# Kernel tuning notes

Measured on AMD Instinct MI355X. Metric: run time of the kernel, lower is better.

Reference implementation:

```python
import jax, jax.numpy as jnp
import numpy as np

N_NODES = 100000


def setup_inputs() -> dict:
    key = jax.random.key(0)
    k1, k2, k3 = jax.random.split(key, 3)
    x = jax.random.normal(k1, (N_NODES, 128), dtype=jnp.float32)
    edge_index = jax.random.randint(k2, (2, 500000), 0, N_NODES, dtype=jnp.int64)
    # GCNConv linear weight (glorot-ish scale) and bias
    W = jax.random.normal(k3, (128, 512), dtype=jnp.float32) * (1.0 / np.sqrt(128.0))
    b = jnp.zeros((512,), dtype=jnp.float32)
    prelu_w = jnp.full((512,), 0.25, dtype=jnp.float32)  # torch PReLU default init
    return {"x": x, "edge_index": edge_index, "W": W, "b": b, "prelu_w": prelu_w}


def reference(x, edge_index, W, b, prelu_w):
    N = x.shape[0]
    # 1) linear transform (GCNConv applies lin before aggregation, bias after)
    h = x @ W  # [N, H]
    # 2) add self-loops
    loops = jnp.arange(N, dtype=edge_index.dtype)
    src = jnp.concatenate([edge_index[0], loops])  # [E+N]
    dst = jnp.concatenate([edge_index[1], loops])
    # 3) symmetric normalization: deg computed on destination nodes
    deg = jax.ops.segment_sum(jnp.ones_like(src, dtype=h.dtype), dst, num_segments=N)
    dinv = jnp.where(deg > 0, deg ** -0.5, 0.0)
    norm = dinv[src] * dinv[dst]  # [E+N]
    # 4) normalized scatter-add aggregation
    msg = h[src] * norm[:, None]  # [E+N, H]
    out = jax.ops.segment_sum(msg, dst, num_segments=N) + b  # [N, H]
    # 5) channel-wise PReLU
    return jnp.where(out >= 0, out, prelu_w * out)
```

## Files before the change

### kernel.cpp

```cpp
#include <hip/hip_runtime.h>


typedef __attribute__((ext_vector_type(8))) short bf16x8_t;
typedef __attribute__((ext_vector_type(4))) float f32x4;

#define N_NODES 100000
#define N_EDGES 500000
#define K_IN    128
#define H_OUT   512
#define MAXDEG  32
#define NEB     1954

static __device__ __forceinline__ unsigned short f2b(float f) {
    unsigned u = __float_as_uint(f);
    u = (u + 0x7FFFu + ((u >> 16) & 1u)) >> 16;
    return (unsigned short)u;
}
static __device__ __forceinline__ float b2lo(unsigned v) {
    return __uint_as_float(v << 16);
}
static __device__ __forceinline__ float b2hi(unsigned v) {
    return __uint_as_float(v & 0xFFFF0000u);
}

__global__ __launch_bounds__(256) void k1(const int* __restrict__ ei,
                                          int* __restrict__ deg,
                                          int* __restrict__ csrp,
                                          const float* __restrict__ W,
                                          unsigned short* __restrict__ Wt) {
    int b = blockIdx.x;
    if (b < NEB) {
        int e = b * 256 + threadIdx.x;
        if (e < N_EDGES) {
            int s = ei[e];
            int d = ei[N_EDGES + e];
            int r = atomicAdd(&deg[d], 1);
            csrp[d * MAXDEG + r] = s;
        }
    } else {
        int i = (b - NEB) * 256 + threadIdx.x;
        int n = i >> 7, k = i & 127;
        Wt[i] = f2b(W[k * H_OUT + n]);
    }
}

__global__ __launch_bounds__(256) void k2(const int* __restrict__ deg,
                                          const float* __restrict__ x,
                                          unsigned* __restrict__ xs) {
    int i = blockIdx.x * 256 + threadIdx.x;
    int row = i >> 6;
    float d = rsqrtf((float)(deg[row] + 1));
    const float2* x2 = (const float2*)x;
    float2 xv = x2[i];
    xs[i] = ((unsigned)f2b(d * xv.y) << 16) | f2b(d * xv.x);
}

__global__ __launch_bounds__(256) void k5(const unsigned* __restrict__ xs,
                                          const int* __restrict__ csrp,
                                          const int* __restrict__ deg,
                                          unsigned* __restrict__ xa) {
    int wave = threadIdx.x >> 6, lane = threadIdx.x & 63;
    int node = blockIdx.x * 4 + wave;
    if (node >= N_NODES) return;

    unsigned sv = xs[(size_t)node * 64 + lane];
    float a0 = b2lo(sv), a1 = b2hi(sv);

    int cnt = __builtin_amdgcn_readfirstlane(deg[node]);
    int base = node * MAXDEG;

    for (int j = 0; j < cnt; j += 8) {
        unsigned v[8];
        #pragma unroll
        for (int t = 0; t < 8; ++t) {
            int valid = (j + t < cnt);
            int idx = valid ? csrp[base + j + t] : 0;
            v[t] = valid ? xs[(size_t)idx * 64 + lane] : 0u;
        }
        #pragma unroll
        for (int t = 0; t < 8; ++t) { a0 += b2lo(v[t]); a1 += b2hi(v[t]); }
    }
    float di = rsqrtf((float)(cnt + 1));
    xa[(size_t)node * 64 + lane] = ((unsigned)f2b(di * a1) << 16) | f2b(di * a0);
}

__global__ __launch_bounds__(256) void k6(const unsigned short* __restrict__ xa,
                                          const unsigned short* __restrict__ Wt,
                                          const float* __restrict__ bias,
                                          const float* __restrict__ pw,
                                          float* __restrict__ out) {
    __shared__ char smem[65536];
    uint4* sA = (uint4*)smem;
    uint4* sB = (uint4*)(smem + 32768);
    float* ep = (float*)smem;

    int orig = blockIdx.x;
    int xcd = orig & 7, loc = orig >> 3;
    int wgid = (xcd < 4 ? xcd * 196 : 784 + (xcd - 4) * 195) + loc;
    const int n0 = (wgid & 3) * 128;
    const int mpair = wgid >> 2;
    const int tid = threadIdx.x;

    const uint4* A4 = (const uint4*)xa;
    const uint4* B4 = (const uint4*)Wt;

    #pragma unroll
    for (int r = 0; r < 8; ++r) {
        int i = tid + r * 256;
        int row = i >> 4, c = i & 15;
        sB[row * 16 + (c ^ (row & 7))] = B4[(size_t)(n0 + row) * 16 + c];
    }

    const int lane = tid & 63, wave = tid >> 6;
    const int wr = wave >> 1, wc = wave & 1;
    const int l16 = lane & 15, lq = lane >> 4;

    float bn[4], pn[4];
    #pragma unroll
    for (int n = 0; n < 4; ++n) {
        int gn = n0 + wc * 64 + n * 16 + l16;
        bn[n] = bias[gn];
        pn[n] = pw[gn];
    }

    for (int half = 0; half < 2; ++half) {
        const int m0 = (mpair * 2 + half) * 128;

        #pragma unroll
        for (int r = 0; r < 8; ++r) {
            int i = tid + r * 256;
            int row = i >> 4, c = i & 15;
            int grow = m0 + row;
            uint4 o = (grow < N_NODES) ? A4[(size_t)grow * 16 + c]
                                       : make_uint4(0u, 0u, 0u, 0u);
            sA[row * 16 + (c ^ (row & 7))] = o;
        }
        __syncthreads();

        f32x4 acc[4][4];
        #pragma unroll
        for (int m = 0; m < 4; ++m)
            #pragma unroll
            for (int n = 0; n < 4; ++n)
                acc[m][n] = (f32x4){0.f, 0.f, 0.f, 0.f};

        #pragma unroll
        for (int kk = 0; kk < 4; ++kk) {
            bf16x8_t av[4], bv[4];
            #pragma unroll
            for (int m = 0; m < 4; ++m) {
                int row = wr * 64 + m * 16 + l16;
                av[m] = __builtin_bit_cast(bf16x8_t, sA[row * 16 + ((kk * 4 + lq) ^ (row & 7))]);
            }
            #pragma unroll
            for (int n = 0; n < 4; ++n) {
                int row = wc * 64 + n * 16 + l16;
                bv[n] = __builtin_bit_cast(bf16x8_t, sB[row * 16 + ((kk * 4 + lq) ^ (row & 7))]);
            }
            #pragma unroll
            for (int m = 0; m < 4; ++m)
                #pragma unroll
                for (int n = 0; n < 4; ++n)
                    acc[m][n] = __builtin_amdgcn_mfma_f32_16x16x32_bf16(av[m], bv[n], acc[m][n], 0, 0, 0);
        }
        __syncthreads();

        #pragma unroll
        for (int h = 0; h < 2; ++h) {
            if (wr == h) {
                #pragma unroll
                for (int m = 0; m < 4; ++m)
                    #pragma unroll
                    for (int r = 0; r < 4; ++r) {
                        int row = m * 16 + lq * 4 + r;
                        #pragma unroll
                        for (int n = 0; n < 4; ++n) {
                            float t = acc[m][n][r] + bn[n];
                            float v = t >= 0.f ? t : pn[n] * t;
                            ep[row * 128 + wc * 64 + n * 16 + l16] = v;
                        }
                    }
            }
            __syncthreads();
            #pragma unroll
            for (int it = 0; it < 8; ++it) {
                int row = it * 8 + (tid >> 5);
                int gm = m0 + h * 64 + row;
                if (gm < N_NODES) {
                    int c4 = tid & 31;
                    f32x4 v = *(const f32x4*)&ep[row * 128 + c4 * 4];
                    __builtin_nontemporal_store(v, (f32x4*)&out[(size_t)gm * H_OUT + n0 + c4 * 4]);
                }
            }
            __syncthreads();
        }
    }
}

extern "C" void kernel_launch(void* const* d_in, const int* in_sizes, int n_in,
                              void* d_out, int out_size, void* d_ws, size_t ws_size,
                              hipStream_t stream) {
    const float* x    = (const float*)d_in[0];
    const int*   ei   = (const int*)d_in[1];
    const float* W    = (const float*)d_in[2];
    const float* bias = (const float*)d_in[3];
    const float* pw   = (const float*)d_in[4];
    float* out = (float*)d_out;

    char* ws = (char*)d_ws;
    size_t off = 0;
    auto alloc = [&](size_t bytes) -> void* {
        void* p = ws + off;
        off += (bytes + 255) & ~(size_t)255;
        return p;
    };
    unsigned*       xs   = (unsigned*)alloc((size_t)N_NODES * K_IN * 2);
    unsigned*       xa   = (unsigned*)alloc((size_t)N_NODES * K_IN * 2);
    unsigned short* Wt   = (unsigned short*)alloc((size_t)K_IN * H_OUT * 2);
    int*            deg  = (int*)alloc((size_t)N_NODES * 4);
    int*            csrp = (int*)alloc((size_t)N_NODES * MAXDEG * 4);
    (void)ws_size; (void)in_sizes; (void)n_in; (void)out_size;

    hipMemsetAsync(deg, 0, (size_t)N_NODES * 4, stream);

    k1 <<<NEB + 256, 256, 0, stream>>>(ei, deg, csrp, W, Wt);
    k2 <<<25000, 256, 0, stream>>>(deg, x, xs);
    k5 <<<(N_NODES + 3) / 4, 256, 0, stream>>>(xs, csrp, deg, xa);
    k6 <<<1564, 256, 0, stream>>>((const unsigned short*)xa,
                                  (const unsigned short*)Wt, bias, pw, out);
}
```

Baseline: 157.7 us.

## Fuse neighbor aggregation into the GEMM kernel via shared-memory A tile

Merges the gather/aggregate kernel and the GEMM+PReLU kernel into one 512-thread kernel. Each block aggregates 128 nodes straight into a swizzled shared-memory A tile, then loops over four 128-column output chunks, reloading the W tile each time. This removes the xa intermediate round trip through global memory and one launch. In exchange there are only 782 blocks, the gather and MFMA phases no longer overlap across kernels, and the epilogue now does scalar non-temporal stores instead of staged 16-byte vector stores.

```diff
diff --git a/kernel.cpp b/kernel.cpp
--- a/kernel.cpp
+++ b/kernel.cpp
@@ -10,6 +10,7 @@
 #define H_OUT   512
 #define MAXDEG  32
 #define NEB     1954
+#define NMT     782
 
 static __device__ __forceinline__ unsigned short f2b(float f) {
     unsigned u = __float_as_uint(f);
@@ -55,145 +56,118 @@
     xs[i] = ((unsigned)f2b(d * xv.y) << 16) | f2b(d * xv.x);
 }
 
-__global__ __launch_bounds__(256) void k5(const unsigned* __restrict__ xs,
-                                          const int* __restrict__ csrp,
-                                          const int* __restrict__ deg,
-                                          unsigned* __restrict__ xa) {
-    int wave = threadIdx.x >> 6, lane = threadIdx.x & 63;
-    int node = blockIdx.x * 4 + wave;
-    if (node >= N_NODES) return;
-
-    unsigned sv = xs[(size_t)node * 64 + lane];
-    float a0 = b2lo(sv), a1 = b2hi(sv);
-
-    int cnt = __builtin_amdgcn_readfirstlane(deg[node]);
-    int base = node * MAXDEG;
-
-    for (int j = 0; j < cnt; j += 8) {
-        unsigned v[8];
-        #pragma unroll
-        for (int t = 0; t < 8; ++t) {
-            int valid = (j + t < cnt);
-            int idx = valid ? csrp[base + j + t] : 0;
-            v[t] = valid ? xs[(size_t)idx * 64 + lane] : 0u;
-        }
-        #pragma unroll
-        for (int t = 0; t < 8; ++t) { a0 += b2lo(v[t]); a1 += b2hi(v[t]); }
-    }
-    float di = rsqrtf((float)(cnt + 1));
-    xa[(size_t)node * 64 + lane] = ((unsigned)f2b(di * a1) << 16) | f2b(di * a0);
-}
-
-__global__ __launch_bounds__(256) void k6(const unsigned short* __restrict__ xa,
-                                          const unsigned short* __restrict__ Wt,
-                                          const float* __restrict__ bias,
-                                          const float* __restrict__ pw,
-                                          float* __restrict__ out) {
+__global__ __launch_bounds__(512) void k56(const unsigned* __restrict__ xs,
+                                           const int* __restrict__ csrp,
+                                           const int* __restrict__ deg,
+                                           const unsigned short* __restrict__ Wt,
+                                           const float* __restrict__ bias,
+                                           const float* __restrict__ pw,
+                                           float* __restrict__ out) {
     __shared__ char smem[65536];
     uint4* sA = (uint4*)smem;
     uint4* sB = (uint4*)(smem + 32768);
-    float* ep = (float*)smem;
 
     int orig = blockIdx.x;
     int xcd = orig & 7, loc = orig >> 3;
-    int wgid = (xcd < 4 ? xcd * 196 : 784 + (xcd - 4) * 195) + loc;
-    const int n0 = (wgid & 3) * 128;
-    const int mpair = wgid >> 2;
+    int wgid = (xcd < 6 ? xcd * 98 : 588 + (xcd - 6) * 97) + loc;
+    const int m0 = wgid * 128;
     const int tid = threadIdx.x;
-
-    const uint4* A4 = (const uint4*)xa;
+    const int wave = tid >> 6, lane = tid & 63;
+
+    unsigned* sAd = (unsigned*)smem;
+    for (int i = 0; i < 16; ++i) {
+        int node = m0 + wave * 16 + i;
+        float a0 = 0.f, a1 = 0.f;
+        int cnt = 0;
+        if (node < N_NODES) {
+            unsigned sv = xs[(size_t)node * 64 + lane];
+            a0 = b2lo(sv); a1 = b2hi(sv);
+            cnt = __builtin_amdgcn_readfirstlane(deg[node]);
+            int base = node * MAXDEG;
+            for (int j = 0; j < cnt; j += 8) {
+                unsigned v[8];
+                #pragma unroll
+                for (int t = 0; t < 8; ++t) {
+                    int valid = (j + t < cnt);
+                    int idx = valid ? csrp[base + j + t] : 0;
+                    v[t] = valid ? xs[(size_t)idx * 64 + lane] : 0u;
+                }
+                #pragma unroll
+                for (int t = 0; t < 8; ++t) { a0 += b2lo(v[t]); a1 += b2hi(v[t]); }
+            }
+        }
+        float di = rsqrtf((float)(cnt + 1));
+        unsigned pk = ((unsigned)f2b(di * a1) << 16) | f2b(di * a0);
+        int row = wave * 16 + i;
+        int c = lane >> 2;
+        sAd[row * 64 + ((c ^ (row & 7)) << 2) + (lane & 3)] = pk;
+    }
+    __syncthreads();
+
     const uint4* B4 = (const uint4*)Wt;
-
-    #pragma unroll
-    for (int r = 0; r < 8; ++r) {
-        int i = tid + r * 256;
-        int row = i >> 4, c = i & 15;
-        sB[row * 16 + (c ^ (row & 7))] = B4[(size_t)(n0 + row) * 16 + c];
-    }
-
-    const int lane = tid & 63, wave = tid >> 6;
-    const int wr = wave >> 1, wc = wave & 1;
+    const int wr = wave >> 2, wc = wave & 3;
     const int l16 = lane & 15, lq = lane >> 4;
 
-    float bn[4], pn[4];
-    #pragma unroll
-    for (int n = 0; n < 4; ++n) {
-        int gn = n0 + wc * 64 + n * 16 + l16;
-        bn[n] = bias[gn];
-        pn[n] = pw[gn];
-    }
-
-    for (int half = 0; half < 2; ++half) {
-        const int m0 = (mpair * 2 + half) * 128;
-
-        #pragma unroll
-        for (int r = 0; r < 8; ++r) {
-            int i = tid + r * 256;
+    for (int nc = 0; nc < 4; ++nc) {
+        #pragma unroll
+        for (int r = 0; r < 4; ++r) {
+            int i = tid + r * 512;
             int row = i >> 4, c = i & 15;
-            int grow = m0 + row;
-            uint4 o = (grow < N_NODES) ? A4[(size_t)grow * 16 + c]
-                                       : make_uint4(0u, 0u, 0u, 0u);
-            sA[row * 16 + (c ^ (row & 7))] = o;
+            sB[row * 16 + (c ^ (row & 7))] = B4[(size_t)(nc * 128 + row) * 16 + c];
         }
         __syncthreads();
 
-        f32x4 acc[4][4];
+        f32x4 acc[4][2];
         #pragma unroll
         for (int m = 0; m < 4; ++m)
             #pragma unroll
-            for (int n = 0; n < 4; ++n)
+            for (int n = 0; n < 2; ++n)
                 acc[m][n] = (f32x4){0.f, 0.f, 0.f, 0.f};
 
         #pragma unroll
         for (int kk = 0; kk < 4; ++kk) {
-            bf16x8_t av[4], bv[4];
+            bf16x8_t av[4], bv[2];
             #pragma unroll
             for (int m = 0; m < 4; ++m) {
                 int row = wr * 64 + m * 16 + l16;
                 av[m] = __builtin_bit_cast(bf16x8_t, sA[row * 16 + ((kk * 4 + lq) ^ (row & 7))]);
             }
             #pragma unroll
-            for (int n = 0; n < 4; ++n) {
-                int row = wc * 64 + n * 16 + l16;
+            for (int n = 0; n < 2; ++n) {
+                int row = wc * 32 + n * 16 + l16;
                 bv[n] = __builtin_bit_cast(bf16x8_t, sB[row * 16 + ((kk * 4 + lq) ^ (row & 7))]);
             }
             #pragma unroll
             for (int m = 0; m < 4; ++m)
                 #pragma unroll
-                for (int n = 0; n < 4; ++n)
+                for (int n = 0; n < 2; ++n)
                     acc[m][n] = __builtin_amdgcn_mfma_f32_16x16x32_bf16(av[m], bv[n], acc[m][n], 0, 0, 0);
         }
+
+        float bn[2], pn[2];
+        #pragma unroll
+        for (int n = 0; n < 2; ++n) {
+            int gn = nc * 128 + wc * 32 + n * 16 + l16;
+            bn[n] = bias[gn];
+            pn[n] = pw[gn];
+        }
+        #pragma unroll
+        for (int m = 0; m < 4; ++m) {
+            #pragma unroll
+            for (int r = 0; r < 4; ++r) {
+                int gm = m0 + wr * 64 + m * 16 + lq * 4 + r;
+                if (gm < N_NODES) {
+                    #pragma unroll
+                    for (int n = 0; n < 2; ++n) {
+                        int gn = nc * 128 + wc * 32 + n * 16 + l16;
+                        float t = acc[m][n][r] + bn[n];
+                        float v = t >= 0.f ? t : pn[n] * t;
+                        __builtin_nontemporal_store(v, &out[(size_t)gm * H_OUT + gn]);
+                    }
+                }
+            }
+        }
         __syncthreads();
-
-        #pragma unroll
-        for (int h = 0; h < 2; ++h) {
-            if (wr == h) {
-                #pragma unroll
-                for (int m = 0; m < 4; ++m)
-                    #pragma unroll
-                    for (int r = 0; r < 4; ++r) {
-                        int row = m * 16 + lq * 4 + r;
-                        #pragma unroll
-                        for (int n = 0; n < 4; ++n) {
-                            float t = acc[m][n][r] + bn[n];
-                            float v = t >= 0.f ? t : pn[n] * t;
-                            ep[row * 128 + wc * 64 + n * 16 + l16] = v;
-                        }
-                    }
-            }
-            __syncthreads();
-            #pragma unroll
-            for (int it = 0; it < 8; ++it) {
-                int row = it * 8 + (tid >> 5);
-                int gm = m0 + h * 64 + row;
-                if (gm < N_NODES) {
-                    int c4 = tid & 31;
-                    f32x4 v = *(const f32x4*)&ep[row * 128 + c4 * 4];
-                    __builtin_nontemporal_store(v, (f32x4*)&out[(size_t)gm * H_OUT + n0 + c4 * 4]);
-                }
-            }
-            __syncthreads();
-        }
     }
 }
 
@@ -215,7 +189,6 @@
         return p;
     };
     unsigned*       xs   = (unsigned*)alloc((size_t)N_NODES * K_IN * 2);
-    unsigned*       xa   = (unsigned*)alloc((size_t)N_NODES * K_IN * 2);
     unsigned short* Wt   = (unsigned short*)alloc((size_t)K_IN * H_OUT * 2);
     int*            deg  = (int*)alloc((size_t)N_NODES * 4);
     int*            csrp = (int*)alloc((size_t)N_NODES * MAXDEG * 4);
@@ -225,7 +198,6 @@
 
     k1 <<<NEB + 256, 256, 0, stream>>>(ei, deg, csrp, W, Wt);
     k2 <<<25000, 256, 0, stream>>>(deg, x, xs);
-    k5 <<<(N_NODES + 3) / 4, 256, 0, stream>>>(xs, csrp, deg, xa);
-    k6 <<<1564, 256, 0, stream>>>((const unsigned short*)xa,
-                                  (const unsigned short*)Wt, bias, pw, out);
-}
+    k56<<<NMT, 512, 0, stream>>>(xs, csrp, deg,
+                                 (const unsigned short*)Wt, bias, pw, out);
+}
```

New measurement: 180.4 us. 14.4% more time.

## Process two nodes per wave in gather and store GEMM output directly

Applied to the files above, without the earlier changes.

The aggregation kernel now handles two destination nodes per wave, loading CSR neighbor indices as int4 vectors and issuing both nodes' gathers together to raise memory-level parallelism. Out-of-range indices are clamped and masked rather than branched on. Separately, the GEMM epilogue drops the LDS staging pass and its barriers and writes each scalar result straight to global memory with nontemporal stores. The direct epilogue produces narrower, less coalesced 4-byte stores (16 contiguous floats per row segment) in place of 16-byte vector stores, and the CSR loop reads padded slots that may hold uninitialized indices, which are clamped before use.

```diff
diff --git a/kernel.cpp b/kernel.cpp
--- a/kernel.cpp
+++ b/kernel.cpp
@@ -60,28 +60,52 @@
                                           const int* __restrict__ deg,
                                           unsigned* __restrict__ xa) {
     int wave = threadIdx.x >> 6, lane = threadIdx.x & 63;
-    int node = blockIdx.x * 4 + wave;
-    if (node >= N_NODES) return;
-
-    unsigned sv = xs[(size_t)node * 64 + lane];
-    float a0 = b2lo(sv), a1 = b2hi(sv);
-
-    int cnt = __builtin_amdgcn_readfirstlane(deg[node]);
-    int base = node * MAXDEG;
-
-    for (int j = 0; j < cnt; j += 8) {
-        unsigned v[8];
+    int n0 = blockIdx.x * 8 + wave * 2;
+    int n1 = n0 + 1;
+
+    unsigned sv0 = xs[(size_t)n0 * 64 + lane];
+    unsigned sv1 = xs[(size_t)n1 * 64 + lane];
+    int cnt0 = __builtin_amdgcn_readfirstlane(deg[n0]);
+    int cnt1 = __builtin_amdgcn_readfirstlane(deg[n1]);
+    float a00 = b2lo(sv0), a01 = b2hi(sv0);
+    float a10 = b2lo(sv1), a11 = b2hi(sv1);
+
+    const int4* cp0 = (const int4*)(csrp + n0 * MAXDEG);
+    const int4* cp1 = (const int4*)(csrp + n1 * MAXDEG);
+    int cmax = cnt0 > cnt1 ? cnt0 : cnt1;
+
+    for (int j = 0; j < cmax; j += 8) {
+        int4 ca0 = cp0[(j >> 2)];
+        int4 cb0 = cp0[(j >> 2) + 1];
+        int4 ca1 = cp1[(j >> 2)];
+        int4 cb1 = cp1[(j >> 2) + 1];
+        unsigned i0[8] = {(unsigned)ca0.x, (unsigned)ca0.y, (unsigned)ca0.z, (unsigned)ca0.w,
+                          (unsigned)cb0.x, (unsigned)cb0.y, (unsigned)cb0.z, (unsigned)cb0.w};
+        unsigned i1[8] = {(unsigned)ca1.x, (unsigned)ca1.y, (unsigned)ca1.z, (unsigned)ca1.w,
+                          (unsigned)cb1.x, (unsigned)cb1.y, (unsigned)cb1.z, (unsigned)cb1.w};
+        unsigned v0[8], v1[8];
         #pragma unroll
         for (int t = 0; t < 8; ++t) {
-            int valid = (j + t < cnt);
-            int idx = valid ? csrp[base + j + t] : 0;
-            v[t] = valid ? xs[(size_t)idx * 64 + lane] : 0u;
-        }
-        #pragma unroll
-        for (int t = 0; t < 8; ++t) { a0 += b2lo(v[t]); a1 += b2hi(v[t]); }
-    }
-    float di = rsqrtf((float)(cnt + 1));
-    xa[(size_t)node * 64 + lane] = ((unsigned)f2b(di * a1) << 16) | f2b(di * a0);
+            unsigned id0 = i0[t] < N_NODES ? i0[t] : 0u;
+            unsigned id1 = i1[t] < N_NODES ? i1[t] : 0u;
+            v0[t] = xs[(size_t)id0 * 64 + lane];
+            v1[t] = xs[(size_t)id1 * 64 + lane];
+        }
+        int rem0 = cnt0 - j, rem1 = cnt1 - j;
+        #pragma unroll
+        for (int t = 0; t < 8; ++t) {
+            unsigned w0 = (t < rem0) ? v0[t] : 0u;
+            unsigned w1 = (t < rem1) ? v1[t] : 0u;
+            a00 += b2lo(w0); a01 += b2hi(w0);
+            a10 += b2lo(w1); a11 += b2hi(w1);
+        }
+    }
+    float d0 = rsqrtf((float)(cnt0 + 1));
+    float d1 = rsqrtf((float)(cnt1 + 1));
+    unsigned p0 = ((unsigned)f2b(d0 * a01) << 16) | f2b(d0 * a00);
+    unsigned p1 = ((unsigned)f2b(d1 * a11) << 16) | f2b(d1 * a10);
+    __builtin_nontemporal_store(p0, &xa[(size_t)n0 * 64 + lane]);
+    __builtin_nontemporal_store(p1, &xa[(size_t)n1 * 64 + lane]);
 }
 
 __global__ __launch_bounds__(256) void k6(const unsigned short* __restrict__ xa,
@@ -92,7 +116,6 @@
     __shared__ char smem[65536];
     uint4* sA = (uint4*)smem;
     uint4* sB = (uint4*)(smem + 32768);
-    float* ep = (float*)smem;
 
     int orig = blockIdx.x;
     int xcd = orig & 7, loc = orig >> 3;
@@ -125,6 +148,7 @@
 
     for (int half = 0; half < 2; ++half) {
         const int m0 = (mpair * 2 + half) * 128;
+        if (half) __syncthreads();
 
         #pragma unroll
         for (int r = 0; r < 8; ++r) {
@@ -163,36 +187,22 @@
                 for (int n = 0; n < 4; ++n)
                     acc[m][n] = __builtin_amdgcn_mfma_f32_16x16x32_bf16(av[m], bv[n], acc[m][n], 0, 0, 0);
         }
-        __syncthreads();
-
-        #pragma unroll
-        for (int h = 0; h < 2; ++h) {
-            if (wr == h) {
-                #pragma unroll
-                for (int m = 0; m < 4; ++m)
+
+        #pragma unroll
+        for (int m = 0; m < 4; ++m) {
+            #pragma unroll
+            for (int r = 0; r < 4; ++r) {
+                int gm = m0 + wr * 64 + m * 16 + lq * 4 + r;
+                if (gm < N_NODES) {
                     #pragma unroll
-                    for (int r = 0; r < 4; ++r) {
-                        int row = m * 16 + lq * 4 + r;
-                        #pragma unroll
-                        for (int n = 0; n < 4; ++n) {
-                            float t = acc[m][n][r] + bn[n];
-                            float v = t >= 0.f ? t : pn[n] * t;
-                            ep[row * 128 + wc * 64 + n * 16 + l16] = v;
-                        }
+                    for (int n = 0; n < 4; ++n) {
+                        int gn = n0 + wc * 64 + n * 16 + l16;
+                        float t = acc[m][n][r] + bn[n];
+                        float v = t >= 0.f ? t : pn[n] * t;
+                        __builtin_nontemporal_store(v, &out[(size_t)gm * H_OUT + gn]);
                     }
-            }
-            __syncthreads();
-            #pragma unroll
-            for (int it = 0; it < 8; ++it) {
-                int row = it * 8 + (tid >> 5);
-                int gm = m0 + h * 64 + row;
-                if (gm < N_NODES) {
-                    int c4 = tid & 31;
-                    f32x4 v = *(const f32x4*)&ep[row * 128 + c4 * 4];
-                    __builtin_nontemporal_store(v, (f32x4*)&out[(size_t)gm * H_OUT + n0 + c4 * 4]);
                 }
             }
-            __syncthreads();
         }
     }
 }
@@ -225,7 +235,7 @@
 
     k1 <<<NEB + 256, 256, 0, stream>>>(ei, deg, csrp, W, Wt);
     k2 <<<25000, 256, 0, stream>>>(deg, x, xs);
-    k5 <<<(N_NODES + 3) / 4, 256, 0, stream>>>(xs, csrp, deg, xa);
+    k5 <<<12500, 256, 0, stream>>>(xs, csrp, deg, xa);
     k6 <<<1564, 256, 0, stream>>>((const unsigned short*)xa,
                                   (const unsigned short*)Wt, bias, pw, out);
 }
```

Measured after the change: 159.0 us. Within noise of the previous version (+0.8%).
